# Optimization experiments

Measured on AMD Instinct MI355X. Metric: run time of the kernel, lower is better.

## Reference

```python
import jax, jax.numpy as jnp
import numpy as np

NU, NT, E, H, NL, NVOC, OUT, HID2 = 100000, 400000, 400000, 128, 3, 10000, 2, 64
EPS = 1e-5


def setup_inputs() -> dict:
    key = jax.random.key(0)
    ks = jax.random.split(key, 20)
    s = 1.0 / np.sqrt(H).astype(np.float32)
    inp = {
        "x_user": jax.random.randint(ks[0], (NU,), 0, NVOC),
        "x_txn": jax.random.randint(ks[1], (NT,), 0, NVOC),
        "ei0_src": jax.random.randint(ks[2], (E,), 0, NU),
        "ei0_dst": jax.random.randint(ks[3], (E,), 0, NT),
        "ei1_src": jax.random.randint(ks[4], (E,), 0, NT),
        "ei1_dst": jax.random.randint(ks[5], (E,), 0, NU),
        "emb_user": jax.random.normal(ks[6], (NVOC, H), jnp.float32),
        "emb_txn": jax.random.normal(ks[7], (NVOC, H), jnp.float32),
        "Wl": jax.random.normal(ks[8], (NL, 2, H, H), jnp.float32) * s,
        "bl": jax.random.normal(ks[9], (NL, 2, H), jnp.float32) * 0.01,
        "Wr": jax.random.normal(ks[10], (NL, 2, H, H), jnp.float32) * s,
        "bn_gamma": jax.random.uniform(ks[11], (NL, 2, H), jnp.float32, 0.5, 1.5),
        "bn_beta": jax.random.normal(ks[12], (NL, 2, H), jnp.float32) * 0.01,
        "bn_mean": jax.random.normal(ks[13], (NL, 2, H), jnp.float32) * 0.01,
        "bn_var": jax.random.uniform(ks[14], (NL, 2, H), jnp.float32, 0.5, 1.5),
        "W1": jax.random.normal(ks[15], (H, HID2), jnp.float32) * s,
        "b1": jax.random.normal(ks[16], (HID2,), jnp.float32) * 0.01,
        "W2": jax.random.normal(ks[17], (HID2, OUT), jnp.float32) * (1.0 / np.sqrt(HID2).astype(np.float32)),
        "b2": jax.random.normal(ks[18], (OUT,), jnp.float32) * 0.01,
    }
    return inp


def _seg_mean(src_feat, src_idx, dst_idx, num_dst):
    # gather per-edge src features, mean-reduce per dst node (SAGEConv aggr='mean')
    msg = src_feat[src_idx]                                        # [E, H]
    tot = jax.ops.segment_sum(msg, dst_idx, num_segments=num_dst)  # [Ndst, H]
    cnt = jax.ops.segment_sum(jnp.ones((dst_idx.shape[0], 1), src_feat.dtype),
                              dst_idx, num_segments=num_dst)
    return tot / jnp.maximum(cnt, 1.0)


def _bn_relu(x, g, b, m, v):
    return jax.nn.relu((x - m) * jax.lax.rsqrt(v + EPS) * g + b)


def reference(x_user, x_txn, ei0_src, ei0_dst, ei1_src, ei1_dst,
              emb_user, emb_txn, Wl, bl, Wr,
              bn_gamma, bn_beta, bn_mean, bn_var, W1, b1, W2, b2):
    h_u = emb_user[x_user]   # [NU, H]
    h_t = emb_txn[x_txn]     # [NT, H]
    for i in range(NL):
        # edge type 0: user -> transaction; edge type 1: transaction -> user
        agg_t = _seg_mean(h_u, ei0_src, ei0_dst, h_t.shape[0])
        agg_u = _seg_mean(h_t, ei1_src, ei1_dst, h_u.shape[0])
        new_t = agg_t @ Wl[i, 0] + bl[i, 0] + h_t @ Wr[i, 0]
        new_u = agg_u @ Wl[i, 1] + bl[i, 1] + h_u @ Wr[i, 1]
        h_u = _bn_relu(new_u, bn_gamma[i, 0], bn_beta[i, 0], bn_mean[i, 0], bn_var[i, 0])
        h_t = _bn_relu(new_t, bn_gamma[i, 1], bn_beta[i, 1], bn_mean[i, 1], bn_var[i, 1])
    h = jnp.concatenate([h_u, h_t], axis=0)            # [NU+NT, H]
    out = jax.nn.relu(h @ W1 + b1) @ W2 + b2           # [NU+NT, OUT]
    return out
```

## Files before the change

### kernel.cpp

```cpp
#include <hip/hip_runtime.h>


#define NUv   100000
#define NTv   400000
#define Ev    400000
#define Hv    128
#define NLv   3
#define HID2v 64
#define EPSv  1e-5f

typedef _Float16 h16;
typedef __attribute__((ext_vector_type(8))) _Float16 f16x8;
typedef __attribute__((ext_vector_type(4))) float    f32x4;

#define WS_NEED (280u * 1024u * 1024u)
__device__ __attribute__((aligned(256))) static unsigned char g_ws[WS_NEED];

__device__ __forceinline__ int imin(int a, int b) { return a < b ? a : b; }
__device__ __forceinline__ int swz(int n, int kbyte) {
  return n * 256 + (kbyte ^ ((n & 7) << 4));
}

__global__ __launch_bounds__(256) void k_count(const int* __restrict__ d0,
                                               const int* __restrict__ d1,
                                               int* __restrict__ c0,
                                               int* __restrict__ c1, int e) {
  int t = blockIdx.x * 256 + threadIdx.x;
  if (t < e) {
    atomicAdd(c0 + d0[t], 1);
    atomicAdd(c1 + d1[t], 1);
  }
}

__global__ __launch_bounds__(256) void k_blocksum(const int* __restrict__ cnt,
                                                  int* __restrict__ bs, int n) {
  __shared__ int red[256];
  int base = blockIdx.x * 2048 + threadIdx.x * 8;
  int s = 0;
#pragma unroll
  for (int j = 0; j < 8; j++) {
    int p = base + j;
    if (p < n) s += cnt[p];
  }
  red[threadIdx.x] = s;
  __syncthreads();
  for (int st = 128; st > 0; st >>= 1) {
    if (threadIdx.x < st) red[threadIdx.x] += red[threadIdx.x + st];
    __syncthreads();
  }
  if (threadIdx.x == 0) bs[blockIdx.x] = red[0];
}

__global__ __launch_bounds__(256) void k_scansmall(int* __restrict__ bs, int g) {
  __shared__ int lds[256];
  int t = threadIdx.x;
  int v = (t < g) ? bs[t] : 0;
  lds[t] = v;
  __syncthreads();
  for (int st = 1; st < 256; st <<= 1) {
    int x = (t >= st) ? lds[t - st] : 0;
    __syncthreads();
    lds[t] += x;
    __syncthreads();
  }
  if (t < g) bs[t] = lds[t] - v;
}

__global__ __launch_bounds__(256) void k_scanfinal(const int* __restrict__ cnt,
                                                   const int* __restrict__ bs,
                                                   int* __restrict__ off,
                                                   int* __restrict__ cur, int n) {
  __shared__ int lds[256];
  int t = threadIdx.x;
  int base = blockIdx.x * 2048 + t * 8;
  int v[8], pre[8];
  int tsum = 0;
#pragma unroll
  for (int j = 0; j < 8; j++) {
    int p = base + j;
    v[j] = (p < n) ? cnt[p] : 0;
    pre[j] = tsum;
    tsum += v[j];
  }
  lds[t] = tsum;
  __syncthreads();
  for (int st = 1; st < 256; st <<= 1) {
    int x = (t >= st) ? lds[t - st] : 0;
    __syncthreads();
    lds[t] += x;
    __syncthreads();
  }
  int texcl = lds[t] - tsum;
  int boff = bs[blockIdx.x];
#pragma unroll
  for (int j = 0; j < 8; j++) {
    int p = base + j;
    if (p < n) {
      int o = boff + texcl + pre[j];
      off[p] = o;
      cur[p] = o;
      if (p == n - 1) off[n] = o + v[j];
    }
  }
}

__global__ __launch_bounds__(256) void k_fill(const int* __restrict__ s0,
                                              const int* __restrict__ d0,
                                              const int* __restrict__ s1,
                                              const int* __restrict__ d1,
                                              int* __restrict__ cur0,
                                              int* __restrict__ cur1,
                                              int* __restrict__ ss0,
                                              int* __restrict__ ss1, int e) {
  int t = blockIdx.x * 256 + threadIdx.x;
  if (t < e) {
    int p = atomicAdd(cur0 + d0[t], 1);
    ss0[p] = s0[t];
    int q = atomicAdd(cur1 + d1[t], 1);
    ss1[q] = s1[t];
  }
}

__global__ __launch_bounds__(256) void k_wt(const float* __restrict__ Wl,
                                            const float* __restrict__ Wr,
                                            const float* __restrict__ W1,
                                            h16* __restrict__ WlT,
                                            h16* __restrict__ WrT,
                                            h16* __restrict__ W1T) {
  int t = blockIdx.x * 256 + threadIdx.x;
  const int NW = NLv * 2 * Hv * Hv;
  if (t < NW) {
    int mat = t / (Hv * Hv);
    int n = (t / Hv) % Hv;
    int k = t % Hv;
    WlT[t] = (h16)Wl[(size_t)mat * Hv * Hv + (size_t)k * Hv + n];
    WrT[t] = (h16)Wr[(size_t)mat * Hv * Hv + (size_t)k * Hv + n];
  } else if (t < NW + HID2v * Hv) {
    int u = t - NW;
    int n = u / Hv;
    int k = u % Hv;
    W1T[u] = (h16)W1[(size_t)k * HID2v + n];
  }
}

__global__ __launch_bounds__(256) void k_bn(const float* __restrict__ g,
                                            const float* __restrict__ b,
                                            const float* __restrict__ m,
                                            const float* __restrict__ v,
                                            float* __restrict__ sc,
                                            float* __restrict__ sh) {
  int t = blockIdx.x * 256 + threadIdx.x;
  if (t < NLv * 2 * Hv) {
    float inv = rsqrtf(v[t] + EPSv);
    float s = g[t] * inv;
    sc[t] = s;
    sh[t] = b[t] - m[t] * s;
  }
}

__global__ __launch_bounds__(256) void k_embed(const int* __restrict__ xu,
                                               const int* __restrict__ xt,
                                               const float* __restrict__ eu,
                                               const float* __restrict__ et,
                                               h16* __restrict__ hu,
                                               h16* __restrict__ ht) {
  int t = blockIdx.x * 256 + threadIdx.x;
  int row = t >> 4;
  int c = (t & 15) * 8;
  if (row >= NUv + NTv) return;
  const float* src;
  h16* dst;
  if (row < NUv) {
    src = eu + (size_t)xu[row] * Hv;
    dst = hu + (size_t)row * Hv;
  } else {
    int r2 = row - NUv;
    src = et + (size_t)xt[r2] * Hv;
    dst = ht + (size_t)r2 * Hv;
  }
  float4 v0 = *(const float4*)(src + c);
  float4 v1 = *(const float4*)(src + c + 4);
  f16x8 o;
  o[0] = (h16)v0.x; o[1] = (h16)v0.y; o[2] = (h16)v0.z; o[3] = (h16)v0.w;
  o[4] = (h16)v1.x; o[5] = (h16)v1.y; o[6] = (h16)v1.z; o[7] = (h16)v1.w;
  *(f16x8*)(dst + c) = o;
}

__global__ __launch_bounds__(512, 6) void k_fused(const h16* __restrict__ SRC,
                                                  const h16* __restrict__ DENSE,
                                                  const int* __restrict__ off,
                                                  const int* __restrict__ ss,
                                                  const h16* __restrict__ BTl,
                                                  const h16* __restrict__ BTr,
                                                  const float* __restrict__ bl,
                                                  const float* __restrict__ sc,
                                                  const float* __restrict__ sh,
                                                  h16* __restrict__ C, int M) {
  __shared__ __align__(16) unsigned char sA[64 * 256];
  __shared__ __align__(16) unsigned char sB[128 * 256];
  int t = threadIdx.x;
  int blockBase = blockIdx.x * 64;
  int l = t & 63;
  int lm = l & 15, lk = l >> 4;
  int rt = (t >> 6) >> 1, nh = (t >> 6) & 1;
  int rowBase = blockBase + rt * 16;

  {
    const h16* bsrc = BTr + t * 32;
    f16x8 b0 = *(const f16x8*)(bsrc + 0);
    f16x8 b1 = *(const f16x8*)(bsrc + 8);
    f16x8 b2 = *(const f16x8*)(bsrc + 16);
    f16x8 b3 = *(const f16x8*)(bsrc + 24);
    int n = t >> 2;
    int kb = (t & 3) * 64;
    *(f16x8*)(sB + swz(n, kb + 0)) = b0;
    *(f16x8*)(sB + swz(n, kb + 16)) = b1;
    *(f16x8*)(sB + swz(n, kb + 32)) = b2;
    *(f16x8*)(sB + swz(n, kb + 48)) = b3;
  }
  int ar = imin(rowBase + lm, M - 1);
  const h16* arow = DENSE + (size_t)ar * Hv;
  f16x8 ad0 = *(const f16x8*)(arow + 0 * 32 + lk * 8);
  f16x8 ad1 = *(const f16x8*)(arow + 1 * 32 + lk * 8);
  f16x8 ad2 = *(const f16x8*)(arow + 2 * 32 + lk * 8);
  f16x8 ad3 = *(const f16x8*)(arow + 3 * 32 + lk * 8);
  __syncthreads();

  {
    int r = t >> 3;
    int cs = (t & 7) * 16;
    float facc[16];
#pragma unroll
    for (int j = 0; j < 16; j++) facc[j] = 0.f;
    int row = blockBase + r;
    if (row < M) {
      int e0 = off[row], e1 = off[row + 1];
      for (int e = e0; e < e1; e += 2) {
        int i0 = ss[e];
        bool v1 = (e + 1) < e1;
        int i1 = v1 ? ss[e + 1] : i0;
        const f16x8* p0 = (const f16x8*)(SRC + (size_t)i0 * Hv + cs);
        const f16x8* p1 = (const f16x8*)(SRC + (size_t)i1 * Hv + cs);
        f16x8 x0 = p0[0], x1 = p0[1];
        f16x8 y0 = p1[0], y1 = p1[1];
        float m1 = v1 ? 1.f : 0.f;
#pragma unroll
        for (int j = 0; j < 8; j++) {
          facc[j] += (float)x0[j];
          facc[8 + j] += (float)x1[j];
          facc[j] = fmaf((float)y0[j], m1, facc[j]);
          facc[8 + j] = fmaf((float)y1[j], m1, facc[8 + j]);
        }
      }
      int deg = e1 - e0;
      float inv = 1.f / (float)(deg > 1 ? deg : 1);
#pragma unroll
      for (int j = 0; j < 16; j++) facc[j] *= inv;
    }
#pragma unroll
    for (int q = 0; q < 2; q++) {
      f16x8 ov;
#pragma unroll
      for (int j = 0; j < 8; j++) ov[j] = (h16)facc[q * 8 + j];
      *(f16x8*)(sA + swz(r, (t & 7) * 32 + q * 16)) = ov;
    }
  }

  f32x4 acc[4];
#pragma unroll
  for (int j = 0; j < 4; j++) acc[j] = (f32x4){0.f, 0.f, 0.f, 0.f};
  {
    f16x8 ads[4] = {ad0, ad1, ad2, ad3};
#pragma unroll
    for (int s = 0; s < 4; s++) {
#pragma unroll
      for (int j = 0; j < 4; j++) {
        int nf = nh * 4 + j;
        f16x8 b = *(const f16x8*)(sB + swz(nf * 16 + lm, s * 64 + lk * 16));
        acc[j] = __builtin_amdgcn_mfma_f32_16x16x32_f16(ads[s], b, acc[j], 0, 0, 0);
      }
    }
  }
  __syncthreads();

  {
    const h16* bsrc = BTl + t * 32;
    f16x8 b0 = *(const f16x8*)(bsrc + 0);
    f16x8 b1 = *(const f16x8*)(bsrc + 8);
    f16x8 b2 = *(const f16x8*)(bsrc + 16);
    f16x8 b3 = *(const f16x8*)(bsrc + 24);
    int n = t >> 2;
    int kb = (t & 3) * 64;
    *(f16x8*)(sB + swz(n, kb + 0)) = b0;
    *(f16x8*)(sB + swz(n, kb + 16)) = b1;
    *(f16x8*)(sB + swz(n, kb + 32)) = b2;
    *(f16x8*)(sB + swz(n, kb + 48)) = b3;
  }
  __syncthreads();

#pragma unroll
  for (int s = 0; s < 4; s++) {
    f16x8 a = *(const f16x8*)(sA + swz(rt * 16 + lm, s * 64 + lk * 16));
#pragma unroll
    for (int j = 0; j < 4; j++) {
      int nf = nh * 4 + j;
      f16x8 b = *(const f16x8*)(sB + swz(nf * 16 + lm, s * 64 + lk * 16));
      acc[j] = __builtin_amdgcn_mfma_f32_16x16x32_f16(a, b, acc[j], 0, 0, 0);
    }
  }
  __syncthreads();

#pragma unroll
  for (int j = 0; j < 4; j++) {
    int col = (nh * 4 + j) * 16 + lm;
    float blv = bl[col], scv = sc[col], shv = sh[col];
#pragma unroll
    for (int r_ = 0; r_ < 4; r_++) {
      float x = fmaf(acc[j][r_] + blv, scv, shv);
      h16 hv = (h16)fmaxf(x, 0.f);
      int rowl = rt * 16 + lk * 4 + r_;
      *(h16*)(sA + swz(rowl, col * 2)) = hv;
    }
  }
  __syncthreads();
  {
    int r = t >> 3;
    int row = blockBase + r;
    if (row < M) {
#pragma unroll
      for (int q = 0; q < 2; q++) {
        f16x8 v = *(const f16x8*)(sA + swz(r, (t & 7) * 32 + q * 16));
        *(f16x8*)(C + (size_t)row * Hv + (t & 7) * 16 + q * 8) = v;
      }
    }
  }
}

__global__ __launch_bounds__(512, 4) void k_mlp(const h16* __restrict__ HU,
                                                const h16* __restrict__ HT,
                                                const h16* __restrict__ W1T,
                                                const float* __restrict__ b1,
                                                const float* __restrict__ W2,
                                                const float* __restrict__ b2,
                                                float* __restrict__ out, int Mtot) {
  __shared__ float y[128][65];
  __shared__ __align__(16) unsigned char sW[64 * 256];
  int t = threadIdx.x;
  int w = t >> 6, l = t & 63;
  int lm = l & 15, lk = l >> 4;

  {
    const h16* src = W1T + t * 16;
    f16x8 w0 = *(const f16x8*)(src + 0);
    f16x8 w1 = *(const f16x8*)(src + 8);
    int n = (t * 16) >> 7;
    int kb = ((t * 16) & 127) * 2;
    *(f16x8*)(sW + swz(n, kb + 0)) = w0;
    *(f16x8*)(sW + swz(n, kb + 16)) = w1;
  }

  int rowBase = blockIdx.x * 128 + w * 16;
  int ar = imin(rowBase + lm, Mtot - 1);
  const h16* arow =
      (ar < NUv) ? (HU + (size_t)ar * Hv) : (HT + (size_t)(ar - NUv) * Hv);
  f16x8 a0 = *(const f16x8*)(arow + 0 * 32 + lk * 8);
  f16x8 a1 = *(const f16x8*)(arow + 1 * 32 + lk * 8);
  f16x8 a2 = *(const f16x8*)(arow + 2 * 32 + lk * 8);
  f16x8 a3 = *(const f16x8*)(arow + 3 * 32 + lk * 8);
  __syncthreads();

  f32x4 acc[4];
#pragma unroll
  for (int nf = 0; nf < 4; nf++) acc[nf] = (f32x4){0.f, 0.f, 0.f, 0.f};
  {
    f16x8 as[4] = {a0, a1, a2, a3};
#pragma unroll
    for (int s = 0; s < 4; s++) {
#pragma unroll
      for (int nf = 0; nf < 4; nf++) {
        f16x8 b = *(const f16x8*)(sW + swz(nf * 16 + lm, s * 64 + lk * 16));
        acc[nf] = __builtin_amdgcn_mfma_f32_16x16x32_f16(as[s], b, acc[nf], 0, 0, 0);
      }
    }
  }
#pragma unroll
  for (int nf = 0; nf < 4; nf++) {
    int col = nf * 16 + lm;
    float b1v = b1[col];
#pragma unroll
    for (int r = 0; r < 4; r++) {
      int rloc = w * 16 + lk * 4 + r;
      y[rloc][col] = fmaxf(acc[nf][r] + b1v, 0.f);
    }
  }
  __syncthreads();
  if (t < 256) {
    int rloc = t >> 1, o = t & 1;
    int row = blockIdx.x * 128 + rloc;
    if (row < Mtot) {
      float sum = b2[o];
#pragma unroll
      for (int k = 0; k < HID2v; k++) sum += y[rloc][k] * W2[k * 2 + o];
      out[(size_t)row * 2 + o] = sum;
    }
  }
}

extern "C" void kernel_launch(void* const* d_in, const int* in_sizes, int n_in,
                              void* d_out, int out_size, void* d_ws, size_t ws_size,
                              hipStream_t stream) {
  (void)in_sizes; (void)n_in; (void)out_size;

  const int* x_user  = (const int*)d_in[0];
  const int* x_txn   = (const int*)d_in[1];
  const int* ei0_src = (const int*)d_in[2];
  const int* ei0_dst = (const int*)d_in[3];
  const int* ei1_src = (const int*)d_in[4];
  const int* ei1_dst = (const int*)d_in[5];
  const float* emb_user = (const float*)d_in[6];
  const float* emb_txn  = (const float*)d_in[7];
  const float* Wl = (const float*)d_in[8];
  const float* bl = (const float*)d_in[9];
  const float* Wr = (const float*)d_in[10];
  const float* bn_g = (const float*)d_in[11];
  const float* bn_b = (const float*)d_in[12];
  const float* bn_m = (const float*)d_in[13];
  const float* bn_v = (const float*)d_in[14];
  const float* W1 = (const float*)d_in[15];
  const float* b1 = (const float*)d_in[16];
  const float* W2 = (const float*)d_in[17];
  const float* b2 = (const float*)d_in[18];
  float* out = (float*)d_out;

  char* wsb;
  if (ws_size >= (size_t)WS_NEED) {
    wsb = (char*)d_ws;
  } else {
    void* sym = nullptr;
    hipGetSymbolAddress(&sym, HIP_SYMBOL(g_ws));
    wsb = (char*)sym;
  }
  size_t o = 0;
  auto alloc = [&](size_t bytes) -> void* {
    o = (o + 255) & ~(size_t)255;
    void* p = wsb + o;
    o += bytes;
    return p;
  };
  h16* hu   = (h16*)alloc((size_t)NUv * Hv * 2);
  h16* ht0  = (h16*)alloc((size_t)NTv * Hv * 2);
  h16* ht1  = (h16*)alloc((size_t)NTv * Hv * 2);
  h16* WlT  = (h16*)alloc((size_t)NLv * 2 * Hv * Hv * 2);
  h16* WrT  = (h16*)alloc((size_t)NLv * 2 * Hv * Hv * 2);
  h16* W1T  = (h16*)alloc((size_t)HID2v * Hv * 2);
  float* bnsc = (float*)alloc((size_t)NLv * 2 * Hv * 4);
  float* bnsh = (float*)alloc((size_t)NLv * 2 * Hv * 4);
  int* off0 = (int*)alloc((size_t)(NTv + 1) * 4);
  int* off1 = (int*)alloc((size_t)(NUv + 1) * 4);
  int* cur0 = (int*)alloc((size_t)NTv * 4);
  int* cur1 = (int*)alloc((size_t)NUv * 4);
  int* ss0  = (int*)alloc((size_t)Ev * 4);
  int* ss1  = (int*)alloc((size_t)Ev * 4);
  int* bs0  = (int*)alloc(256 * 4);
  int* bs1  = (int*)alloc(256 * 4);

  const int G_E    = (Ev + 255) / 256;
  const int G_BS0  = (NTv + 2047) / 2048;
  const int G_BS1  = (NUv + 2047) / 2048;
  const int G_EMB  = ((NUv + NTv) * 16 + 255) / 256;
  const int G_WT   = (NLv * 2 * Hv * Hv + HID2v * Hv + 255) / 256;
  const int G_T    = (NTv + 63) / 64;
  const int G_U    = (NUv + 63) / 64;
  const int G_MLP  = (NUv + NTv + 127) / 128;

  hipMemsetAsync(cur0, 0, (size_t)NTv * 4, stream);
  hipMemsetAsync(cur1, 0, (size_t)NUv * 4, stream);
  k_count<<<G_E, 256, 0, stream>>>(ei0_dst, ei1_dst, cur0, cur1, Ev);
  k_blocksum<<<G_BS0, 256, 0, stream>>>(cur0, bs0, NTv);
  k_blocksum<<<G_BS1, 256, 0, stream>>>(cur1, bs1, NUv);
  k_scansmall<<<1, 256, 0, stream>>>(bs0, G_BS0);
  k_scansmall<<<1, 256, 0, stream>>>(bs1, G_BS1);
  k_scanfinal<<<G_BS0, 256, 0, stream>>>(cur0, bs0, off0, cur0, NTv);
  k_scanfinal<<<G_BS1, 256, 0, stream>>>(cur1, bs1, off1, cur1, NUv);
  k_fill<<<G_E, 256, 0, stream>>>(ei0_src, ei0_dst, ei1_src, ei1_dst,
                                  cur0, cur1, ss0, ss1, Ev);

  k_wt<<<G_WT, 256, 0, stream>>>(Wl, Wr, W1, WlT, WrT, W1T);
  k_bn<<<3, 256, 0, stream>>>(bn_g, bn_b, bn_m, bn_v, bnsc, bnsh);

  k_embed<<<G_EMB, 256, 0, stream>>>(x_user, x_txn, emb_user, emb_txn, hu, ht0);

  h16* ht_cur = ht0; h16* ht_nxt = ht1;
  for (int i = 0; i < NLv; i++) {
    const h16* WlT0 = WlT + (size_t)(i * 2 + 0) * Hv * Hv;
    const h16* WlT1 = WlT + (size_t)(i * 2 + 1) * Hv * Hv;
    const h16* WrT0 = WrT + (size_t)(i * 2 + 0) * Hv * Hv;
    const h16* WrT1 = WrT + (size_t)(i * 2 + 1) * Hv * Hv;
    const float* bl0 = bl + (size_t)(i * 2 + 0) * Hv;
    const float* bl1 = bl + (size_t)(i * 2 + 1) * Hv;
    const float* sc0 = bnsc + (size_t)(i * 2 + 0) * Hv;
    const float* sh0 = bnsh + (size_t)(i * 2 + 0) * Hv;
    const float* sc1 = bnsc + (size_t)(i * 2 + 1) * Hv;
    const float* sh1 = bnsh + (size_t)(i * 2 + 1) * Hv;

    k_fused<<<G_T, 512, 0, stream>>>(hu, ht_cur, off0, ss0, WlT0, WrT0,
                                     bl0, sc1, sh1, ht_nxt, NTv);
    k_fused<<<G_U, 512, 0, stream>>>(ht_cur, hu, off1, ss1, WlT1, WrT1,
                                     bl1, sc0, sh0, hu, NUv);
    h16* tmp = ht_cur; ht_cur = ht_nxt; ht_nxt = tmp;
  }

  k_mlp<<<G_MLP, 512, 0, stream>>>(hu, ht_cur, W1T, b1, W2, b2, out, NUv + NTv);
}
```

Before: 713.8 us.

## Parallelize segment-mean over edges with LDS float atomics per block

The fused SAGE layer kernel now spreads the neighbor aggregation across the block's edge range instead of giving each destination row to 8 threads. Edge source indices are staged in LDS, each edge's row is found by binary search over the block's offsets, and features are accumulated with shared-memory float atomicAdd into an fp32 tile that is scaled by inverse degree when loaded into the MFMA. This targets load imbalance from skewed degrees and serial per-row gather loops. In exchange it uses more LDS (occupancy hint drops from 6 to 4 blocks), adds atomic contention, and makes the summation order nondeterministic.

```diff
diff --git a/kernel.cpp b/kernel.cpp
--- a/kernel.cpp
+++ b/kernel.cpp
@@ -8,6 +8,7 @@
 #define NLv   3
 #define HID2v 64
 #define EPSv  1e-5f
+#define SECAP 2048
 
 typedef _Float16 h16;
 typedef __attribute__((ext_vector_type(8))) _Float16 f16x8;
@@ -186,7 +187,7 @@
   *(f16x8*)(dst + c) = o;
 }
 
-__global__ __launch_bounds__(512, 6) void k_fused(const h16* __restrict__ SRC,
+__global__ __launch_bounds__(512, 4) void k_fused(const h16* __restrict__ SRC,
                                                   const h16* __restrict__ DENSE,
                                                   const int* __restrict__ off,
                                                   const int* __restrict__ ss,
@@ -196,15 +197,33 @@
                                                   const float* __restrict__ sc,
                                                   const float* __restrict__ sh,
                                                   h16* __restrict__ C, int M) {
-  __shared__ __align__(16) unsigned char sA[64 * 256];
   __shared__ __align__(16) unsigned char sB[128 * 256];
+  __shared__ __align__(16) float sAf[64 * 128];
+  __shared__ int   sE[SECAP];
+  __shared__ int   sO[65];
+  __shared__ float sInv[64];
+
   int t = threadIdx.x;
-  int blockBase = blockIdx.x * 64;
+  int base = blockIdx.x * 64;
   int l = t & 63;
   int lm = l & 15, lk = l >> 4;
   int rt = (t >> 6) >> 1, nh = (t >> 6) & 1;
-  int rowBase = blockBase + rt * 16;
-
+  int rowBase = base + rt * 16;
+
+  int mEnd = imin(base + 64, M);
+  int e0 = off[base];
+  int e1 = off[mEnd];
+  int eblk = e1 - e0;
+
+  if (t <= 64) sO[t] = off[imin(base + t, M)];
+  if (t < 64) {
+    int rr = base + t;
+    int d = (rr < M) ? (off[rr + 1] - off[rr]) : 0;
+    sInv[t] = 1.f / (float)(d > 1 ? d : 1);
+  }
+#pragma unroll
+  for (int j = 0; j < 4; j++)
+    *(f32x4*)(&sAf[(t + j * 512) * 4]) = (f32x4){0.f, 0.f, 0.f, 0.f};
   {
     const h16* bsrc = BTr + t * 32;
     f16x8 b0 = *(const f16x8*)(bsrc + 0);
@@ -218,6 +237,7 @@
     *(f16x8*)(sB + swz(n, kb + 32)) = b2;
     *(f16x8*)(sB + swz(n, kb + 48)) = b3;
   }
+  for (int i = t; i < eblk && i < SECAP; i += 512) sE[i] = ss[e0 + i];
   int ar = imin(rowBase + lm, M - 1);
   const h16* arow = DENSE + (size_t)ar * Hv;
   f16x8 ad0 = *(const f16x8*)(arow + 0 * 32 + lk * 8);
@@ -226,44 +246,22 @@
   f16x8 ad3 = *(const f16x8*)(arow + 3 * 32 + lk * 8);
   __syncthreads();
 
-  {
-    int r = t >> 3;
-    int cs = (t & 7) * 16;
-    float facc[16];
-#pragma unroll
-    for (int j = 0; j < 16; j++) facc[j] = 0.f;
-    int row = blockBase + r;
-    if (row < M) {
-      int e0 = off[row], e1 = off[row + 1];
-      for (int e = e0; e < e1; e += 2) {
-        int i0 = ss[e];
-        bool v1 = (e + 1) < e1;
-        int i1 = v1 ? ss[e + 1] : i0;
-        const f16x8* p0 = (const f16x8*)(SRC + (size_t)i0 * Hv + cs);
-        const f16x8* p1 = (const f16x8*)(SRC + (size_t)i1 * Hv + cs);
-        f16x8 x0 = p0[0], x1 = p0[1];
-        f16x8 y0 = p1[0], y1 = p1[1];
-        float m1 = v1 ? 1.f : 0.f;
-#pragma unroll
-        for (int j = 0; j < 8; j++) {
-          facc[j] += (float)x0[j];
-          facc[8 + j] += (float)x1[j];
-          facc[j] = fmaf((float)y0[j], m1, facc[j]);
-          facc[8 + j] = fmaf((float)y1[j], m1, facc[8 + j]);
-        }
-      }
-      int deg = e1 - e0;
-      float inv = 1.f / (float)(deg > 1 ? deg : 1);
-#pragma unroll
-      for (int j = 0; j < 16; j++) facc[j] *= inv;
-    }
-#pragma unroll
-    for (int q = 0; q < 2; q++) {
-      f16x8 ov;
-#pragma unroll
-      for (int j = 0; j < 8; j++) ov[j] = (h16)facc[q * 8 + j];
-      *(f16x8*)(sA + swz(r, (t & 7) * 32 + q * 16)) = ov;
-    }
+  int slice = t & 7;
+  int csbyte = slice * 64;
+  int ei0 = t >> 3;
+  f16x8 g0a, g0b;
+  int grow0 = -1;
+  if (ei0 < eblk) {
+    int srcIdx = (ei0 < SECAP) ? sE[ei0] : ss[e0 + ei0];
+    const h16* sp = SRC + (size_t)srcIdx * Hv + slice * 16;
+    g0a = *(const f16x8*)(sp);
+    g0b = *(const f16x8*)(sp + 8);
+    int ge = e0 + ei0;
+    int lo = 0;
+#pragma unroll
+    for (int st = 32; st >= 1; st >>= 1)
+      if (lo + st <= 63 && sO[lo + st] <= ge) lo += st;
+    grow0 = lo;
   }
 
   f32x4 acc[4];
@@ -281,35 +279,93 @@
       }
     }
   }
+
+  if (grow0 >= 0) {
+    float vals[16];
+#pragma unroll
+    for (int j = 0; j < 8; j++) {
+      vals[j] = (float)g0a[j];
+      vals[8 + j] = (float)g0b[j];
+    }
+    int sw = (grow0 & 7) << 4;
+    int wbase = grow0 * 128;
+#pragma unroll
+    for (int j = 0; j < 16; j++) {
+      int jj = (j + t) & 15;
+      int byte = ((csbyte + ((jj >> 2) << 4)) ^ sw) + ((jj & 3) << 2);
+      atomicAdd(&sAf[wbase + (byte >> 2)], vals[jj]);
+    }
+  }
+
+  for (int ei = ei0 + 64; ei < eblk; ei += 64) {
+    int srcIdx = (ei < SECAP) ? sE[ei] : ss[e0 + ei];
+    const h16* sp = SRC + (size_t)srcIdx * Hv + slice * 16;
+    f16x8 ga = *(const f16x8*)(sp);
+    f16x8 gb = *(const f16x8*)(sp + 8);
+    int ge = e0 + ei;
+    int lo = 0;
+#pragma unroll
+    for (int st = 32; st >= 1; st >>= 1)
+      if (lo + st <= 63 && sO[lo + st] <= ge) lo += st;
+    float vals[16];
+#pragma unroll
+    for (int j = 0; j < 8; j++) {
+      vals[j] = (float)ga[j];
+      vals[8 + j] = (float)gb[j];
+    }
+    int sw = (lo & 7) << 4;
+    int wbase = lo * 128;
+#pragma unroll
+    for (int j = 0; j < 16; j++) {
+      int jj = (j + t) & 15;
+      int byte = ((csbyte + ((jj >> 2) << 4)) ^ sw) + ((jj & 3) << 2);
+      atomicAdd(&sAf[wbase + (byte >> 2)], vals[jj]);
+    }
+  }
+
+  const h16* bsrc2 = BTl + t * 32;
+  f16x8 bw0 = *(const f16x8*)(bsrc2 + 0);
+  f16x8 bw1 = *(const f16x8*)(bsrc2 + 8);
+  f16x8 bw2 = *(const f16x8*)(bsrc2 + 16);
+  f16x8 bw3 = *(const f16x8*)(bsrc2 + 24);
   __syncthreads();
 
   {
-    const h16* bsrc = BTl + t * 32;
-    f16x8 b0 = *(const f16x8*)(bsrc + 0);
-    f16x8 b1 = *(const f16x8*)(bsrc + 8);
-    f16x8 b2 = *(const f16x8*)(bsrc + 16);
-    f16x8 b3 = *(const f16x8*)(bsrc + 24);
     int n = t >> 2;
     int kb = (t & 3) * 64;
-    *(f16x8*)(sB + swz(n, kb + 0)) = b0;
-    *(f16x8*)(sB + swz(n, kb + 16)) = b1;
-    *(f16x8*)(sB + swz(n, kb + 32)) = b2;
-    *(f16x8*)(sB + swz(n, kb + 48)) = b3;
-  }
-  __syncthreads();
-
-#pragma unroll
-  for (int s = 0; s < 4; s++) {
-    f16x8 a = *(const f16x8*)(sA + swz(rt * 16 + lm, s * 64 + lk * 16));
-#pragma unroll
-    for (int j = 0; j < 4; j++) {
-      int nf = nh * 4 + j;
-      f16x8 b = *(const f16x8*)(sB + swz(nf * 16 + lm, s * 64 + lk * 16));
-      acc[j] = __builtin_amdgcn_mfma_f32_16x16x32_f16(a, b, acc[j], 0, 0, 0);
-    }
-  }
-  __syncthreads();
-
+    *(f16x8*)(sB + swz(n, kb + 0)) = bw0;
+    *(f16x8*)(sB + swz(n, kb + 16)) = bw1;
+    *(f16x8*)(sB + swz(n, kb + 32)) = bw2;
+    *(f16x8*)(sB + swz(n, kb + 48)) = bw3;
+  }
+  __syncthreads();
+
+  {
+    int row = rt * 16 + lm;
+    float inv = sInv[row];
+    int sw = (row & 7) << 4;
+    const unsigned char* rbase = (const unsigned char*)sAf + row * 512;
+#pragma unroll
+    for (int s = 0; s < 4; s++) {
+      int cb = s * 128 + lk * 32;
+      f32x4 f0 = *(const f32x4*)(rbase + ((cb) ^ sw));
+      f32x4 f1 = *(const f32x4*)(rbase + ((cb + 16) ^ sw));
+      f16x8 a;
+      a[0] = (h16)(f0[0] * inv); a[1] = (h16)(f0[1] * inv);
+      a[2] = (h16)(f0[2] * inv); a[3] = (h16)(f0[3] * inv);
+      a[4] = (h16)(f1[0] * inv); a[5] = (h16)(f1[1] * inv);
+      a[6] = (h16)(f1[2] * inv); a[7] = (h16)(f1[3] * inv);
+#pragma unroll
+      for (int j = 0; j < 4; j++) {
+        int nf = nh * 4 + j;
+        f16x8 b = *(const f16x8*)(sB + swz(nf * 16 + lm, s * 64 + lk * 16));
+        acc[j] = __builtin_amdgcn_mfma_f32_16x16x32_f16(a, b, acc[j], 0, 0, 0);
+      }
+    }
+  }
+  __syncthreads();
+
+  unsigned char* sOut = (unsigned char*)sAf;
 #pragma unroll
   for (int j = 0; j < 4; j++) {
     int col = (nh * 4 + j) * 16 + lm;
@@ -319,18 +375,20 @@
       float x = fmaf(acc[j][r_] + blv, scv, shv);
       h16 hv = (h16)fmaxf(x, 0.f);
       int rowl = rt * 16 + lk * 4 + r_;
-      *(h16*)(sA + swz(rowl, col * 2)) = hv;
-    }
-  }
-  __syncthreads();
-  {
-    int r = t >> 3;
-    int row = blockBase + r;
+      *(h16*)(sOut + swz(rowl, col * 2)) = hv;
+    }
+  }
+  __syncthreads();
+
+  if (t < 256) {
+    int r = t >> 2;
+    int cs = (t & 3) * 64;
+    int row = base + r;
     if (row < M) {
 #pragma unroll
-      for (int q = 0; q < 2; q++) {
-        f16x8 v = *(const f16x8*)(sA + swz(r, (t & 7) * 32 + q * 16));
-        *(f16x8*)(C + (size_t)row * Hv + (t & 7) * 16 + q * 8) = v;
+      for (int q = 0; q < 4; q++) {
+        f16x8 v = *(const f16x8*)(sOut + swz(r, cs + q * 16));
+        *(f16x8*)(C + (size_t)row * Hv + (cs >> 1) + q * 8) = v;
       }
     }
   }
```

Measured after the change: 2.233 ms. 3.13x slower.

## Make fused SAGE layer kernel persistent with both weight matrices resident in LDS

Applied to the files above, without the earlier changes.

The fused aggregation plus GEMM kernel becomes a persistent grid of 512 blocks that loops over 64-row tiles. Both the Wr and Wl transposed weights are loaded into a 64KB shared buffer once per block, instead of being reloaded for every tile with an extra barrier in between. The epilogue now writes each fp16 output element straight to global memory instead of staging the tile in LDS for coalesced 16-byte stores. The trade-offs are higher LDS use per block, which lowers occupancy for the latency-bound gather, and narrow, scattered output stores.

```diff
diff --git a/kernel.cpp b/kernel.cpp
--- a/kernel.cpp
+++ b/kernel.cpp
@@ -19,6 +19,9 @@
 __device__ __forceinline__ int imin(int a, int b) { return a < b ? a : b; }
 __device__ __forceinline__ int swz(int n, int kbyte) {
   return n * 256 + (kbyte ^ ((n & 7) << 4));
+}
+__device__ __forceinline__ int swzB(int n, int kbyte) {
+  return n * 512 + (kbyte ^ ((n & 7) << 4));
 }
 
 __global__ __launch_bounds__(256) void k_count(const int* __restrict__ d0,
@@ -186,7 +189,7 @@
   *(f16x8*)(dst + c) = o;
 }
 
-__global__ __launch_bounds__(512, 6) void k_fused(const h16* __restrict__ SRC,
+__global__ __launch_bounds__(512, 4) void k_fused(const h16* __restrict__ SRC,
                                                   const h16* __restrict__ DENSE,
                                                   const int* __restrict__ off,
                                                   const int* __restrict__ ss,
@@ -196,143 +199,131 @@
                                                   const float* __restrict__ sc,
                                                   const float* __restrict__ sh,
                                                   h16* __restrict__ C, int M) {
+  __shared__ __align__(16) unsigned char sB[128 * 512];
   __shared__ __align__(16) unsigned char sA[64 * 256];
-  __shared__ __align__(16) unsigned char sB[128 * 256];
+
   int t = threadIdx.x;
-  int blockBase = blockIdx.x * 64;
   int l = t & 63;
   int lm = l & 15, lk = l >> 4;
-  int rt = (t >> 6) >> 1, nh = (t >> 6) & 1;
-  int rowBase = blockBase + rt * 16;
+  int w = t >> 6;
+  int rg = w >> 1, cg = w & 1;
 
   {
-    const h16* bsrc = BTr + t * 32;
-    f16x8 b0 = *(const f16x8*)(bsrc + 0);
-    f16x8 b1 = *(const f16x8*)(bsrc + 8);
-    f16x8 b2 = *(const f16x8*)(bsrc + 16);
-    f16x8 b3 = *(const f16x8*)(bsrc + 24);
     int n = t >> 2;
     int kb = (t & 3) * 64;
-    *(f16x8*)(sB + swz(n, kb + 0)) = b0;
-    *(f16x8*)(sB + swz(n, kb + 16)) = b1;
-    *(f16x8*)(sB + swz(n, kb + 32)) = b2;
-    *(f16x8*)(sB + swz(n, kb + 48)) = b3;
-  }
-  int ar = imin(rowBase + lm, M - 1);
-  const h16* arow = DENSE + (size_t)ar * Hv;
-  f16x8 ad0 = *(const f16x8*)(arow + 0 * 32 + lk * 8);
-  f16x8 ad1 = *(const f16x8*)(arow + 1 * 32 + lk * 8);
-  f16x8 ad2 = *(const f16x8*)(arow + 2 * 32 + lk * 8);
-  f16x8 ad3 = *(const f16x8*)(arow + 3 * 32 + lk * 8);
+    const h16* sr = BTr + t * 32;
+    f16x8 r0 = *(const f16x8*)(sr + 0);
+    f16x8 r1 = *(const f16x8*)(sr + 8);
+    f16x8 r2 = *(const f16x8*)(sr + 16);
+    f16x8 r3 = *(const f16x8*)(sr + 24);
+    const h16* sl = BTl + t * 32;
+    f16x8 l0 = *(const f16x8*)(sl + 0);
+    f16x8 l1 = *(const f16x8*)(sl + 8);
+    f16x8 l2 = *(const f16x8*)(sl + 16);
+    f16x8 l3 = *(const f16x8*)(sl + 24);
+    *(f16x8*)(sB + swzB(n, kb + 0)) = r0;
+    *(f16x8*)(sB + swzB(n, kb + 16)) = r1;
+    *(f16x8*)(sB + swzB(n, kb + 32)) = r2;
+    *(f16x8*)(sB + swzB(n, kb + 48)) = r3;
+    *(f16x8*)(sB + swzB(n, 256 + kb + 0)) = l0;
+    *(f16x8*)(sB + swzB(n, 256 + kb + 16)) = l1;
+    *(f16x8*)(sB + swzB(n, 256 + kb + 32)) = l2;
+    *(f16x8*)(sB + swzB(n, 256 + kb + 48)) = l3;
+  }
   __syncthreads();
 
-  {
-    int r = t >> 3;
-    int cs = (t & 7) * 16;
-    float facc[16];
-#pragma unroll
-    for (int j = 0; j < 16; j++) facc[j] = 0.f;
-    int row = blockBase + r;
-    if (row < M) {
-      int e0 = off[row], e1 = off[row + 1];
-      for (int e = e0; e < e1; e += 2) {
-        int i0 = ss[e];
-        bool v1 = (e + 1) < e1;
-        int i1 = v1 ? ss[e + 1] : i0;
-        const f16x8* p0 = (const f16x8*)(SRC + (size_t)i0 * Hv + cs);
-        const f16x8* p1 = (const f16x8*)(SRC + (size_t)i1 * Hv + cs);
-        f16x8 x0 = p0[0], x1 = p0[1];
-        f16x8 y0 = p1[0], y1 = p1[1];
-        float m1 = v1 ? 1.f : 0.f;
-#pragma unroll
-        for (int j = 0; j < 8; j++) {
-          facc[j] += (float)x0[j];
-          facc[8 + j] += (float)x1[j];
-          facc[j] = fmaf((float)y0[j], m1, facc[j]);
-          facc[8 + j] = fmaf((float)y1[j], m1, facc[8 + j]);
+  int nTiles = (M + 63) / 64;
+  for (int tile = blockIdx.x; tile < nTiles; tile += gridDim.x) {
+    int base = tile * 64;
+
+    int ar = imin(base + rg * 16 + lm, M - 1);
+    const h16* arow = DENSE + (size_t)ar * Hv;
+    f16x8 ad0 = *(const f16x8*)(arow + 0 * 32 + lk * 8);
+    f16x8 ad1 = *(const f16x8*)(arow + 1 * 32 + lk * 8);
+    f16x8 ad2 = *(const f16x8*)(arow + 2 * 32 + lk * 8);
+    f16x8 ad3 = *(const f16x8*)(arow + 3 * 32 + lk * 8);
+
+    {
+      int r = t >> 3;
+      int cs = (t & 7) * 16;
+      float facc[16];
+#pragma unroll
+      for (int j = 0; j < 16; j++) facc[j] = 0.f;
+      int row = base + r;
+      if (row < M) {
+        int e0 = off[row], e1 = off[row + 1];
+        for (int e = e0; e < e1; e += 2) {
+          int i0 = ss[e];
+          bool v1 = (e + 1) < e1;
+          int i1 = v1 ? ss[e + 1] : i0;
+          const f16x8* p0 = (const f16x8*)(SRC + (size_t)i0 * Hv + cs);
+          const f16x8* p1 = (const f16x8*)(SRC + (size_t)i1 * Hv + cs);
+          f16x8 x0 = p0[0], x1 = p0[1];
+          f16x8 y0 = p1[0], y1 = p1[1];
+          float m1 = v1 ? 1.f : 0.f;
+#pragma unroll
+          for (int j = 0; j < 8; j++) {
+            facc[j] += (float)x0[j];
+            facc[8 + j] += (float)x1[j];
+            facc[j] = fmaf((float)y0[j], m1, facc[j]);
+            facc[8 + j] = fmaf((float)y1[j], m1, facc[8 + j]);
+          }
+        }
+        int deg = e1 - e0;
+        float inv = 1.f / (float)(deg > 1 ? deg : 1);
+#pragma unroll
+        for (int j = 0; j < 16; j++) facc[j] *= inv;
+      }
+#pragma unroll
+      for (int q = 0; q < 2; q++) {
+        f16x8 ov;
+#pragma unroll
+        for (int j = 0; j < 8; j++) ov[j] = (h16)facc[q * 8 + j];
+        *(f16x8*)(sA + swz(r, cs * 2 + q * 16)) = ov;
+      }
+    }
+    __syncthreads();
+
+    f32x4 acc[4];
+#pragma unroll
+    for (int j = 0; j < 4; j++) acc[j] = (f32x4){0.f, 0.f, 0.f, 0.f};
+    {
+      f16x8 ads[4] = {ad0, ad1, ad2, ad3};
+#pragma unroll
+      for (int s = 0; s < 4; s++) {
+#pragma unroll
+        for (int j = 0; j < 4; j++) {
+          int n = (cg * 4 + j) * 16 + lm;
+          f16x8 b = *(const f16x8*)(sB + swzB(n, s * 64 + lk * 16));
+          acc[j] = __builtin_amdgcn_mfma_f32_16x16x32_f16(ads[s], b, acc[j], 0, 0, 0);
         }
       }
-      int deg = e1 - e0;
-      float inv = 1.f / (float)(deg > 1 ? deg : 1);
-#pragma unroll
-      for (int j = 0; j < 16; j++) facc[j] *= inv;
-    }
-#pragma unroll
-    for (int q = 0; q < 2; q++) {
-      f16x8 ov;
-#pragma unroll
-      for (int j = 0; j < 8; j++) ov[j] = (h16)facc[q * 8 + j];
-      *(f16x8*)(sA + swz(r, (t & 7) * 32 + q * 16)) = ov;
-    }
-  }
-
-  f32x4 acc[4];
-#pragma unroll
-  for (int j = 0; j < 4; j++) acc[j] = (f32x4){0.f, 0.f, 0.f, 0.f};
-  {
-    f16x8 ads[4] = {ad0, ad1, ad2, ad3};
-#pragma unroll
-    for (int s = 0; s < 4; s++) {
-#pragma unroll
-      for (int j = 0; j < 4; j++) {
-        int nf = nh * 4 + j;
-        f16x8 b = *(const f16x8*)(sB + swz(nf * 16 + lm, s * 64 + lk * 16));
-        acc[j] = __builtin_amdgcn_mfma_f32_16x16x32_f16(ads[s], b, acc[j], 0, 0, 0);
+#pragma unroll
+      for (int s = 0; s < 4; s++) {
+        f16x8 a = *(const f16x8*)(sA + swz(rg * 16 + lm, s * 64 + lk * 16));
+#pragma unroll
+        for (int j = 0; j < 4; j++) {
+          int n = (cg * 4 + j) * 16 + lm;
+          f16x8 b = *(const f16x8*)(sB + swzB(n, 256 + s * 64 + lk * 16));
+          acc[j] = __builtin_amdgcn_mfma_f32_16x16x32_f16(a, b, acc[j], 0, 0, 0);
+        }
       }
     }
-  }
-  __syncthreads();
-
-  {
-    const h16* bsrc = BTl + t * 32;
-    f16x8 b0 = *(const f16x8*)(bsrc + 0);
-    f16x8 b1 = *(const f16x8*)(bsrc + 8);
-    f16x8 b2 = *(const f16x8*)(bsrc + 16);
-    f16x8 b3 = *(const f16x8*)(bsrc + 24);
-    int n = t >> 2;
-    int kb = (t & 3) * 64;
-    *(f16x8*)(sB + swz(n, kb + 0)) = b0;
-    *(f16x8*)(sB + swz(n, kb + 16)) = b1;
-    *(f16x8*)(sB + swz(n, kb + 32)) = b2;
-    *(f16x8*)(sB + swz(n, kb + 48)) = b3;
-  }
-  __syncthreads();
-
-#pragma unroll
-  for (int s = 0; s < 4; s++) {
-    f16x8 a = *(const f16x8*)(sA + swz(rt * 16 + lm, s * 64 + lk * 16));
+
 #pragma unroll
     for (int j = 0; j < 4; j++) {
-      int nf = nh * 4 + j;
-      f16x8 b = *(const f16x8*)(sB + swz(nf * 16 + lm, s * 64 + lk * 16));
-      acc[j] = __builtin_amdgcn_mfma_f32_16x16x32_f16(a, b, acc[j], 0, 0, 0);
-    }
-  }
-  __syncthreads();
-
-#pragma unroll
-  for (int j = 0; j < 4; j++) {
-    int col = (nh * 4 + j) * 16 + lm;
-    float blv = bl[col], scv = sc[col], shv = sh[col];
-#pragma unroll
-    for (int r_ = 0; r_ < 4; r_++) {
-      float x = fmaf(acc[j][r_] + blv, scv, shv);
-      h16 hv = (h16)fmaxf(x, 0.f);
-      int rowl = rt * 16 + lk * 4 + r_;
-      *(h16*)(sA + swz(rowl, col * 2)) = hv;
-    }
-  }
-  __syncthreads();
-  {
-    int r = t >> 3;
-    int row = blockBase + r;
-    if (row < M) {
-#pragma unroll
-      for (int q = 0; q < 2; q++) {
-        f16x8 v = *(const f16x8*)(sA + swz(r, (t & 7) * 32 + q * 16));
-        *(f16x8*)(C + (size_t)row * Hv + (t & 7) * 16 + q * 8) = v;
+      int col = (cg * 4 + j) * 16 + lm;
+      float blv = bl[col], scv = sc[col], shv = sh[col];
+#pragma unroll
+      for (int r_ = 0; r_ < 4; r_++) {
+        int row = base + rg * 16 + lk * 4 + r_;
+        if (row < M) {
+          float x = fmaf(acc[j][r_] + blv, scv, shv);
+          C[(size_t)row * Hv + col] = (h16)fmaxf(x, 0.f);
+        }
       }
     }
+    __syncthreads();
   }
 }
 
@@ -469,8 +460,7 @@
   const int G_BS1  = (NUv + 2047) / 2048;
   const int G_EMB  = ((NUv + NTv) * 16 + 255) / 256;
   const int G_WT   = (NLv * 2 * Hv * Hv + HID2v * Hv + 255) / 256;
-  const int G_T    = (NTv + 63) / 64;
-  const int G_U    = (NUv + 63) / 64;
+  const int G_F    = 512;
   const int G_MLP  = (NUv + NTv + 127) / 128;
 
   hipMemsetAsync(cur0, 0, (size_t)NTv * 4, stream);
@@ -503,9 +493,9 @@
     const float* sc1 = bnsc + (size_t)(i * 2 + 1) * Hv;
     const float* sh1 = bnsh + (size_t)(i * 2 + 1) * Hv;
 
-    k_fused<<<G_T, 512, 0, stream>>>(hu, ht_cur, off0, ss0, WlT0, WrT0,
+    k_fused<<<G_F, 512, 0, stream>>>(hu, ht_cur, off0, ss0, WlT0, WrT0,
                                      bl0, sc1, sh1, ht_nxt, NTv);
-    k_fused<<<G_U, 512, 0, stream>>>(ht_cur, hu, off1, ss1, WlT1, WrT1,
+    k_fused<<<G_F, 512, 0, stream>>>(ht_cur, hu, off1, ss1, WlT1, WrT1,
                                      bl1, sc0, sh0, hu, NUv);
     h16* tmp = ht_cur; ht_cur = ht_nxt; ht_nxt = tmp;
   }
```

After: 660.4 us. -7.5%, faster.
